# Kernel tuning notes

Measured on AMD Instinct MI355X. Metric: run time of the kernel, lower is better.

The kernel has to match this reference:

```python
import jax, jax.numpy as jnp
import numpy as np

B, T, C = 2, 2048, 1024
H, DK, OUT = 16, 64, 1024


def setup_inputs() -> dict:
    key = jax.random.key(0)
    k1, k2, k3, k4, k5 = jax.random.split(key, 5)
    glorot_qkv = (2.0 / (C + H * DK)) ** 0.5  # glorot_normal stddev for [C,H,DK]
    glorot_o = (2.0 / (H * DK + OUT)) ** 0.5
    return {
        "x": jax.random.normal(k1, (B, T, C), dtype=jnp.float32),
        "query_mat": jax.random.normal(k2, (C, H, DK), dtype=jnp.float32) * glorot_qkv,
        "key_mat": jax.random.normal(k3, (C, H, DK), dtype=jnp.float32) * glorot_qkv,
        "value_mat": jax.random.normal(k4, (C, H, DK), dtype=jnp.float32) * glorot_qkv,
        "linear_m1": jax.random.normal(k5, (H * DK, OUT), dtype=jnp.float32) * glorot_o,
    }


def reference(x, query_mat, key_mat, value_mat, linear_m1):
    # x: [B,T,C]; projections: [C,H,DK]
    q = jnp.einsum('btc,chd->bhtd', x, query_mat)
    k = jnp.einsum('btc,chd->bhtd', x, key_mat)
    v = jnp.einsum('btc,chd->bhtd', x, value_mat)
    d_k = query_mat.shape[-1]
    # NOTE: faithful to source, which MULTIPLIES by sqrt(d_k)
    w = jnp.einsum('bhtd,bhzd->bhtz', q, k) * (d_k ** 0.5)
    t = w.shape[-1]
    causal = jnp.tril(jnp.ones((t, t), dtype=bool))  # [T,T]
    w = jnp.where(causal, w, -jnp.inf)
    w = jax.nn.softmax(w, axis=-1)
    # dropout inactive (training=False)
    o = jnp.einsum('bhtz,bhzd->bhtd', w, v)
    o = o.transpose(0, 2, 1, 3).reshape(o.shape[0], o.shape[2], -1)  # [B,T,H*DK]
    return jnp.einsum('btc,cz->btz', o, linear_m1)
```

## Files before the change

kernel.cpp:

```cpp
#include <hip/hip_runtime.h>


typedef unsigned short u16;
typedef unsigned int u32;
typedef unsigned long long u64;
typedef __attribute__((ext_vector_type(8))) short bf16x8;
typedef __attribute__((ext_vector_type(4))) float f32x4;

__device__ inline u16 f2bf(float f) {
  union { float f; unsigned u; } v; v.f = f;
  unsigned r = v.u + 0x7FFFu + ((v.u >> 16) & 1u);
  return (u16)(r >> 16);
}
__device__ inline float bf2f(u16 h) {
  union { unsigned u; float f; } v; v.u = ((unsigned)h) << 16;
  return v.f;
}
__device__ inline void glds16(const u16* g, u16* s) {
  __builtin_amdgcn_global_load_lds(
      (const __attribute__((address_space(1))) u32*)g,
      (__attribute__((address_space(3))) u32*)s, 16, 0, 0);
}
#define MFMA __builtin_amdgcn_mfma_f32_16x16x32_bf16

__global__ __launch_bounds__(256) void prep(
    const float* __restrict__ x,
    const float* __restrict__ wq, const float* __restrict__ wk,
    const float* __restrict__ wv, const float* __restrict__ wo,
    u16* __restrict__ Xh, u16* __restrict__ Xl,
    u16* __restrict__ Wqh, u16* __restrict__ Wql,
    u16* __restrict__ Wkh, u16* __restrict__ Wkl,
    u16* __restrict__ Wvt, u16* __restrict__ Wot) {
  const int z = blockIdx.z;
  const int tid = threadIdx.x;
  if (z == 0) {
    const int bid = blockIdx.y * 32 + blockIdx.x;
#pragma unroll
    for (int k = 0; k < 4; k++) {
      int i = bid * 4096 + k * 1024 + tid * 4;
      float4 v = *(const float4*)(x + i);
      ushort4 h, l;
      h.x = f2bf(v.x); l.x = f2bf(v.x - bf2f(h.x));
      h.y = f2bf(v.y); l.y = f2bf(v.y - bf2f(h.y));
      h.z = f2bf(v.z); l.z = f2bf(v.z - bf2f(h.z));
      h.w = f2bf(v.w); l.w = f2bf(v.w - bf2f(h.w));
      *(ushort4*)(Xh + i) = h;
      *(ushort4*)(Xl + i) = l;
    }
    return;
  }
  __shared__ float tile[32][33];
  const float* W = (z == 1) ? wq : (z == 2) ? wk : (z == 3) ? wv : wo;
  const int bx = blockIdx.x * 32, by = blockIdx.y * 32;
  const int tx = tid & 31, ty = tid >> 5;
#pragma unroll
  for (int j = 0; j < 32; j += 8)
    tile[ty + j][tx] = W[(size_t)(by + ty + j) * 1024 + bx + tx];
  __syncthreads();
  if (z <= 2) {
    u16* Th = (z == 1) ? Wqh : Wkh;
    u16* Tl = (z == 1) ? Wql : Wkl;
#pragma unroll
    for (int j = 0; j < 32; j += 8) {
      float v = tile[tx][ty + j];
      u16 h = f2bf(v);
      size_t idx = (size_t)(bx + ty + j) * 1024 + by + tx;
      Th[idx] = h;
      Tl[idx] = f2bf(v - bf2f(h));
    }
  } else {
    u16* T = (z == 3) ? Wvt : Wot;
#pragma unroll
    for (int j = 0; j < 32; j += 8)
      T[(size_t)(bx + ty + j) * 1024 + by + tx] = f2bf(tile[tx][ty + j]);
  }
}

__global__ __launch_bounds__(256) void gemm_qkv(
    const u16* __restrict__ Xh, const u16* __restrict__ Xl,
    const u16* __restrict__ Wqh, const u16* __restrict__ Wql,
    const u16* __restrict__ Wkh, const u16* __restrict__ Wkl,
    const u16* __restrict__ Wvt,
    u16* __restrict__ Qh, u16* __restrict__ Ql,
    u16* __restrict__ Kh, u16* __restrict__ Kl,
    u16* __restrict__ Vt) {
  __shared__ u16 S[4][128][32];
  const int K = 1024;
  const int z = blockIdx.z;
  const bool split = (z < 2);
  const u16* Bh = (z == 0) ? Wqh : (z == 1) ? Wkh : Wvt;
  const u16* Bl = (z == 0) ? Wql : Wkl;
  const int tid = threadIdx.x;
  const int lane = tid & 63, wv = tid >> 6;
  const int quad = lane >> 4, lc = lane & 15;
  const int m0 = blockIdx.y * 128, n0 = blockIdx.x * 128;
  const int wm = (wv >> 1) * 64, wn = (wv & 1) * 64;
  const int lrow = lane >> 2, lk = (lane & 3) * 8;
  const u16* a0p = Xh + (size_t)(m0 + wv * 32 + lrow) * K + lk;
  const u16* a1p = a0p + 16 * K;
  const u16* al0p = Xl + (size_t)(m0 + wv * 32 + lrow) * K + lk;
  const u16* al1p = al0p + 16 * K;
  const u16* b0p = Bh + (size_t)(n0 + wv * 32 + lrow) * K + lk;
  const u16* b1p = b0p + 16 * K;
  const u16* bl0p = split ? (Bl + (size_t)(n0 + wv * 32 + lrow) * K + lk) : b0p;
  const u16* bl1p = bl0p + 16 * K;
  u16* sA0 = &S[0][wv * 32][0];      u16* sA1 = &S[0][wv * 32 + 16][0];
  u16* sAl0 = &S[1][wv * 32][0];     u16* sAl1 = &S[1][wv * 32 + 16][0];
  u16* sB0 = &S[2][wv * 32][0];      u16* sB1 = &S[2][wv * 32 + 16][0];
  u16* sBl0 = &S[3][wv * 32][0];     u16* sBl1 = &S[3][wv * 32 + 16][0];
  f32x4 acc[4][4];
#pragma unroll
  for (int i = 0; i < 4; i++)
#pragma unroll
    for (int j = 0; j < 4; j++) acc[i][j] = (f32x4){0.f, 0.f, 0.f, 0.f};
  for (int kc = 0; kc < K; kc += 32) {
    __syncthreads();
    glds16(a0p + kc, sA0); glds16(a1p + kc, sA1);
    glds16(b0p + kc, sB0); glds16(b1p + kc, sB1);
    if (split) {
      glds16(al0p + kc, sAl0); glds16(al1p + kc, sAl1);
      glds16(bl0p + kc, sBl0); glds16(bl1p + kc, sBl1);
    }
    __syncthreads();
    bf16x8 ah[4], al[4];
#pragma unroll
    for (int mt = 0; mt < 4; mt++)
      ah[mt] = *(const bf16x8*)&S[0][wm + mt * 16 + lc][quad * 8];
    if (split) {
#pragma unroll
      for (int mt = 0; mt < 4; mt++)
        al[mt] = *(const bf16x8*)&S[1][wm + mt * 16 + lc][quad * 8];
    }
#pragma unroll
    for (int nt = 0; nt < 4; nt++) {
      bf16x8 bfh = *(const bf16x8*)&S[2][wn + nt * 16 + lc][quad * 8];
#pragma unroll
      for (int mt = 0; mt < 4; mt++)
        acc[mt][nt] = MFMA(ah[mt], bfh, acc[mt][nt], 0, 0, 0);
      if (split) {
        bf16x8 bfl = *(const bf16x8*)&S[3][wn + nt * 16 + lc][quad * 8];
#pragma unroll
        for (int mt = 0; mt < 4; mt++) {
          acc[mt][nt] = MFMA(ah[mt], bfl, acc[mt][nt], 0, 0, 0);
          acc[mt][nt] = MFMA(al[mt], bfh, acc[mt][nt], 0, 0, 0);
        }
      }
    }
  }
  const int rb = quad * 4;
  if (z == 2) {
#pragma unroll
    for (int mt = 0; mt < 4; mt++)
#pragma unroll
      for (int nt = 0; nt < 4; nt++)
#pragma unroll
        for (int r = 0; r < 4; r++) {
          int m = m0 + wm + mt * 16 + rb + r, n = n0 + wn + nt * 16 + lc;
          int b = m >> 11, t = m & 2047, h = n >> 6, d = n & 63;
          Vt[((size_t)(b * 16 + h) * 64 + d) * 2048 + t] = f2bf(acc[mt][nt][r]);
        }
  } else {
    u16* Ch = (z == 0) ? Qh : Kh;
    u16* Cl = (z == 0) ? Ql : Kl;
    const float scale = (z == 0) ? 8.0f : 1.0f;
#pragma unroll
    for (int mt = 0; mt < 4; mt++)
#pragma unroll
      for (int nt = 0; nt < 4; nt++)
#pragma unroll
        for (int r = 0; r < 4; r++) {
          int m = m0 + wm + mt * 16 + rb + r, n = n0 + wn + nt * 16 + lc;
          int b = m >> 11, t = m & 2047, h = n >> 6, d = n & 63;
          float v = acc[mt][nt][r] * scale;
          u16 hv = f2bf(v);
          size_t idx = ((size_t)(b * 16 + h) * 2048 + t) * 64 + d;
          Ch[idx] = hv;
          Cl[idx] = f2bf(v - bf2f(hv));
        }
  }
}

__global__ __launch_bounds__(256) void gemm_out(const u16* __restrict__ A,
                                                const u16* __restrict__ Bt,
                                                float* __restrict__ C) {
  __shared__ u16 Sa[64][32], Sb[128][32];
  const int K = 1024, N = 1024;
  const int tid = threadIdx.x;
  const int lane = tid & 63, wv = tid >> 6;
  const int quad = lane >> 4, lc = lane & 15;
  const int m0 = blockIdx.y * 64, n0 = blockIdx.x * 128;
  const int wm = (wv >> 1) * 32, wn = (wv & 1) * 64;
  const int lrow = lane >> 2, lk = (lane & 3) * 8;
  const u16* ap = A + (size_t)(m0 + wv * 16 + lrow) * K + lk;
  const u16* b0p = Bt + (size_t)(n0 + wv * 32 + lrow) * K + lk;
  const u16* b1p = b0p + 16 * K;
  u16* sA = &Sa[wv * 16][0];
  u16* sB0 = &Sb[wv * 32][0];
  u16* sB1 = &Sb[wv * 32 + 16][0];
  f32x4 acc[2][4];
#pragma unroll
  for (int i = 0; i < 2; i++)
#pragma unroll
    for (int j = 0; j < 4; j++) acc[i][j] = (f32x4){0.f, 0.f, 0.f, 0.f};
  for (int kc = 0; kc < K; kc += 32) {
    __syncthreads();
    glds16(ap + kc, sA);
    glds16(b0p + kc, sB0);
    glds16(b1p + kc, sB1);
    __syncthreads();
    bf16x8 ah[2];
#pragma unroll
    for (int mt = 0; mt < 2; mt++)
      ah[mt] = *(const bf16x8*)&Sa[wm + mt * 16 + lc][quad * 8];
#pragma unroll
    for (int nt = 0; nt < 4; nt++) {
      bf16x8 bfh = *(const bf16x8*)&Sb[wn + nt * 16 + lc][quad * 8];
#pragma unroll
      for (int mt = 0; mt < 2; mt++)
        acc[mt][nt] = MFMA(ah[mt], bfh, acc[mt][nt], 0, 0, 0);
    }
  }
#pragma unroll
  for (int mt = 0; mt < 2; mt++)
#pragma unroll
    for (int nt = 0; nt < 4; nt++)
#pragma unroll
      for (int r = 0; r < 4; r++)
        C[(size_t)(m0 + wm + mt * 16 + quad * 4 + r) * N + n0 + wn + nt * 16 + lc] =
            acc[mt][nt][r];
}

__global__ __launch_bounds__(256, 2) void attn(const u16* __restrict__ Qh,
                                               const u16* __restrict__ Ql,
                                               const u16* __restrict__ Kh,
                                               const u16* __restrict__ Kl,
                                               const u16* __restrict__ Vt,
                                               u16* __restrict__ O16) {
  __shared__ u16 Khs[2][64][64], Kls[2][64][64], Vs[2][64][64];
  __shared__ u16 Ps[4][16][72];
  const int tid = threadIdx.x;
  const int lane = tid & 63, w = tid >> 6;
  const int quad = lane >> 4, lc = lane & 15;
  const int i = blockIdx.x;
  const int bh = i & 31;
  const int qb = 31 - (i >> 5);
  const int ng = qb + 1;
  const int tq = qb * 64 + w * 16 + lc;
  const size_t kbase = (size_t)bh * 2048 * 64;
  const size_t vbase = (size_t)bh * 64 * 2048;
  const size_t qoff = kbase + (size_t)tq * 64 + quad * 8;
  bf16x8 qh0 = *(const bf16x8*)(Qh + qoff);
  bf16x8 qh1 = *(const bf16x8*)(Qh + qoff + 32);
  bf16x8 ql0 = *(const bf16x8*)(Ql + qoff);
  bf16x8 ql1 = *(const bf16x8*)(Ql + qoff + 32);
  const int srow = lane >> 3;
  const int scol = (lane & 7) ^ srow;
  const u16* kg0 = Kh + kbase + (size_t)(w * 16 + srow) * 64 + scol * 8;
  const u16* lg0 = Kl + kbase + (size_t)(w * 16 + srow) * 64 + scol * 8;
  const u16* vg0 = Vt + vbase + (size_t)(w * 16 + srow) * 2048 + scol * 8;

  float mi = -3.0e38f, li = 0.f;
  f32x4 o[4];
#pragma unroll
  for (int d = 0; d < 4; d++) o[d] = (f32x4){0.f, 0.f, 0.f, 0.f};
  const int rx = lc & 7;

  {
    glds16(kg0, &Khs[0][w * 16][0]); glds16(kg0 + 8 * 64, &Khs[0][w * 16 + 8][0]);
    glds16(lg0, &Kls[0][w * 16][0]); glds16(lg0 + 8 * 64, &Kls[0][w * 16 + 8][0]);
    glds16(vg0, &Vs[0][w * 16][0]);  glds16(vg0 + 8 * 2048, &Vs[0][w * 16 + 8][0]);
  }
  for (int g = 0; g < ng; g++) {
    const int buf = g & 1;
    const int z0 = g * 64;
    __syncthreads();
    if (g + 1 < ng) {
      const int zn = (g + 1) * 64;
      const int nb = buf ^ 1;
      glds16(kg0 + (size_t)zn * 64, &Khs[nb][w * 16][0]);
      glds16(kg0 + (size_t)zn * 64 + 8 * 64, &Khs[nb][w * 16 + 8][0]);
      glds16(lg0 + (size_t)zn * 64, &Kls[nb][w * 16][0]);
      glds16(lg0 + (size_t)zn * 64 + 8 * 64, &Kls[nb][w * 16 + 8][0]);
      glds16(vg0 + zn, &Vs[nb][w * 16][0]);
      glds16(vg0 + zn + 8 * 2048, &Vs[nb][w * 16 + 8][0]);
    }
    f32x4 s[4];
#pragma unroll
    for (int tt = 0; tt < 4; tt++) {
      const int R = tt * 16 + lc;
      bf16x8 kh0 = *(const bf16x8*)&Khs[buf][R][(quad ^ rx) * 8];
      bf16x8 kh1 = *(const bf16x8*)&Khs[buf][R][((4 + quad) ^ rx) * 8];
      bf16x8 kl0 = *(const bf16x8*)&Kls[buf][R][(quad ^ rx) * 8];
      bf16x8 kl1 = *(const bf16x8*)&Kls[buf][R][((4 + quad) ^ rx) * 8];
      f32x4 sv = (f32x4){0.f, 0.f, 0.f, 0.f};
      sv = MFMA(kh0, qh0, sv, 0, 0, 0);
      sv = MFMA(kh1, qh1, sv, 0, 0, 0);
      sv = MFMA(kh0, ql0, sv, 0, 0, 0);
      sv = MFMA(kh1, ql1, sv, 0, 0, 0);
      sv = MFMA(kl0, qh0, sv, 0, 0, 0);
      sv = MFMA(kl1, qh1, sv, 0, 0, 0);
      s[tt] = sv;
    }
    if (g == ng - 1) {
#pragma unroll
      for (int tt = 0; tt < 4; tt++)
#pragma unroll
        for (int r = 0; r < 4; r++)
          if (z0 + tt * 16 + quad * 4 + r > tq) s[tt][r] = -3.0e38f;
    }
    float smax = -3.0e38f;
#pragma unroll
    for (int tt = 0; tt < 4; tt++)
#pragma unroll
      for (int r = 0; r < 4; r++) smax = fmaxf(smax, s[tt][r]);
    smax = fmaxf(smax, __shfl_xor(smax, 16));
    smax = fmaxf(smax, __shfl_xor(smax, 32));
    float mnew = fmaxf(mi, smax);
    float alpha = __expf(mi - mnew);
    mi = mnew;
    float rs = 0.f;
#pragma unroll
    for (int tt = 0; tt < 4; tt++) {
      union { u16 h[4]; u64 d; } pk;
#pragma unroll
      for (int r = 0; r < 4; r++) {
        float p = __expf(s[tt][r] - mnew);
        rs += p;
        pk.h[r] = f2bf(p);
      }
      *(u64*)&Ps[w][lc][tt * 16 + quad * 4] = pk.d;
    }
    li = li * alpha + rs;
#pragma unroll
    for (int d = 0; d < 4; d++) o[d] *= alpha;
    bf16x8 pf0 = *(const bf16x8*)&Ps[w][lc][quad * 8];
    bf16x8 pf1 = *(const bf16x8*)&Ps[w][lc][32 + quad * 8];
#pragma unroll
    for (int dd = 0; dd < 4; dd++) {
      const int R = dd * 16 + lc;
      bf16x8 va0 = *(const bf16x8*)&Vs[buf][R][(quad ^ rx) * 8];
      bf16x8 va1 = *(const bf16x8*)&Vs[buf][R][((4 + quad) ^ rx) * 8];
      o[dd] = MFMA(va0, pf0, o[dd], 0, 0, 0);
      o[dd] = MFMA(va1, pf1, o[dd], 0, 0, 0);
    }
  }
  li += __shfl_xor(li, 16);
  li += __shfl_xor(li, 32);
  const float rli = 1.0f / li;
  const int b = bh >> 4, hh = bh & 15;
  const size_t obase = ((size_t)(b * 2048 + tq)) * 1024 + hh * 64 + quad * 4;
#pragma unroll
  for (int dd = 0; dd < 4; dd++) {
    ushort4 ov;
    ov.x = f2bf(o[dd][0] * rli);
    ov.y = f2bf(o[dd][1] * rli);
    ov.z = f2bf(o[dd][2] * rli);
    ov.w = f2bf(o[dd][3] * rli);
    *(ushort4*)&O16[obase + dd * 16] = ov;
  }
}

extern "C" void kernel_launch(void* const* d_in, const int* in_sizes, int n_in,
                              void* d_out, int out_size, void* d_ws, size_t ws_size,
                              hipStream_t stream) {
  const float* x  = (const float*)d_in[0];
  const float* wq = (const float*)d_in[1];
  const float* wk = (const float*)d_in[2];
  const float* wv = (const float*)d_in[3];
  const float* wo = (const float*)d_in[4];

  char* w = (char*)d_ws;
  const size_t MB = 1u << 20;
  u16* Xh  = (u16*)(w + 0 * MB);
  u16* Xl  = (u16*)(w + 8 * MB);
  u16* Wqh = (u16*)(w + 16 * MB);
  u16* Wql = (u16*)(w + 18 * MB);
  u16* Wkh = (u16*)(w + 20 * MB);
  u16* Wkl = (u16*)(w + 22 * MB);
  u16* Wvt = (u16*)(w + 24 * MB);
  u16* Wot = (u16*)(w + 26 * MB);
  u16* Qhb = (u16*)(w + 28 * MB);
  u16* Qlb = (u16*)(w + 36 * MB);
  u16* Khb = (u16*)(w + 44 * MB);
  u16* Klb = (u16*)(w + 52 * MB);
  u16* Vtb = (u16*)(w + 60 * MB);
  u16* O16 = (u16*)(w + 0 * MB);

  hipLaunchKernelGGL(prep, dim3(32, 32, 5), dim3(256), 0, stream,
                     x, wq, wk, wv, wo, Xh, Xl, Wqh, Wql, Wkh, Wkl, Wvt, Wot);

  hipLaunchKernelGGL(gemm_qkv, dim3(8, 32, 3), dim3(256), 0, stream,
                     Xh, Xl, Wqh, Wql, Wkh, Wkl, Wvt, Qhb, Qlb, Khb, Klb, Vtb);

  hipLaunchKernelGGL(attn, dim3(1024), dim3(256), 0, stream,
                     Qhb, Qlb, Khb, Klb, Vtb, O16);

  hipLaunchKernelGGL(gemm_out, dim3(8, 64), dim3(256), 0, stream, O16, Wot, (float*)d_out);
}
```

Before: 214.3 us.

## Pair causal query blocks per workgroup and software-pipeline PV behind QK

Each attention workgroup now handles two query blocks, qb and 31-qb, so every block does the same amount of causal work and the grid halves to 512. The PV MFMA for the previous key tile is deferred and issued after the current tile's QK MFMAs, with V fragments held in registers. This is meant to overlap softmax latency with matrix work and to remove the tail imbalance of causal scheduling. It raises register pressure through the held V fragments and leaves fewer workgroups to spread across the CUs.

```diff
diff --git a/kernel.cpp b/kernel.cpp
--- a/kernel.cpp
+++ b/kernel.cpp
@@ -241,122 +241,146 @@
   const int tid = threadIdx.x;
   const int lane = tid & 63, w = tid >> 6;
   const int quad = lane >> 4, lc = lane & 15;
-  const int i = blockIdx.x;
-  const int bh = i & 31;
-  const int qb = 31 - (i >> 5);
-  const int ng = qb + 1;
-  const int tq = qb * 64 + w * 16 + lc;
+  const int j = blockIdx.x;
+  const int bh = j & 31;
+  const int pr = j >> 5;
   const size_t kbase = (size_t)bh * 2048 * 64;
   const size_t vbase = (size_t)bh * 64 * 2048;
-  const size_t qoff = kbase + (size_t)tq * 64 + quad * 8;
-  bf16x8 qh0 = *(const bf16x8*)(Qh + qoff);
-  bf16x8 qh1 = *(const bf16x8*)(Qh + qoff + 32);
-  bf16x8 ql0 = *(const bf16x8*)(Ql + qoff);
-  bf16x8 ql1 = *(const bf16x8*)(Ql + qoff + 32);
   const int srow = lane >> 3;
   const int scol = (lane & 7) ^ srow;
+  const int rx = lc & 7;
   const u16* kg0 = Kh + kbase + (size_t)(w * 16 + srow) * 64 + scol * 8;
   const u16* lg0 = Kl + kbase + (size_t)(w * 16 + srow) * 64 + scol * 8;
   const u16* vg0 = Vt + vbase + (size_t)(w * 16 + srow) * 2048 + scol * 8;
-
-  float mi = -3.0e38f, li = 0.f;
-  f32x4 o[4];
-#pragma unroll
-  for (int d = 0; d < 4; d++) o[d] = (f32x4){0.f, 0.f, 0.f, 0.f};
-  const int rx = lc & 7;
-
-  {
+  const int b = bh >> 4, hh = bh & 15;
+
+#pragma unroll 1
+  for (int sb = 0; sb < 2; sb++) {
+    const int qb = sb ? pr : 31 - pr;
+    const int ng = qb + 1;
+    const int tq = qb * 64 + w * 16 + lc;
+    const size_t qoff = kbase + (size_t)tq * 64 + quad * 8;
+    bf16x8 qh0 = *(const bf16x8*)(Qh + qoff);
+    bf16x8 qh1 = *(const bf16x8*)(Qh + qoff + 32);
+    bf16x8 ql0 = *(const bf16x8*)(Ql + qoff);
+    bf16x8 ql1 = *(const bf16x8*)(Ql + qoff + 32);
+    float mi = -3.0e38f, li = 0.f;
+    f32x4 o[4];
+#pragma unroll
+    for (int d = 0; d < 4; d++) o[d] = (f32x4){0.f, 0.f, 0.f, 0.f};
+    bf16x8 vprev[4][2];
+    __syncthreads();
     glds16(kg0, &Khs[0][w * 16][0]); glds16(kg0 + 8 * 64, &Khs[0][w * 16 + 8][0]);
     glds16(lg0, &Kls[0][w * 16][0]); glds16(lg0 + 8 * 64, &Kls[0][w * 16 + 8][0]);
     glds16(vg0, &Vs[0][w * 16][0]);  glds16(vg0 + 8 * 2048, &Vs[0][w * 16 + 8][0]);
-  }
-  for (int g = 0; g < ng; g++) {
-    const int buf = g & 1;
-    const int z0 = g * 64;
-    __syncthreads();
-    if (g + 1 < ng) {
-      const int zn = (g + 1) * 64;
-      const int nb = buf ^ 1;
-      glds16(kg0 + (size_t)zn * 64, &Khs[nb][w * 16][0]);
-      glds16(kg0 + (size_t)zn * 64 + 8 * 64, &Khs[nb][w * 16 + 8][0]);
-      glds16(lg0 + (size_t)zn * 64, &Kls[nb][w * 16][0]);
-      glds16(lg0 + (size_t)zn * 64 + 8 * 64, &Kls[nb][w * 16 + 8][0]);
-      glds16(vg0 + zn, &Vs[nb][w * 16][0]);
-      glds16(vg0 + zn + 8 * 2048, &Vs[nb][w * 16 + 8][0]);
-    }
-    f32x4 s[4];
-#pragma unroll
-    for (int tt = 0; tt < 4; tt++) {
-      const int R = tt * 16 + lc;
-      bf16x8 kh0 = *(const bf16x8*)&Khs[buf][R][(quad ^ rx) * 8];
-      bf16x8 kh1 = *(const bf16x8*)&Khs[buf][R][((4 + quad) ^ rx) * 8];
-      bf16x8 kl0 = *(const bf16x8*)&Kls[buf][R][(quad ^ rx) * 8];
-      bf16x8 kl1 = *(const bf16x8*)&Kls[buf][R][((4 + quad) ^ rx) * 8];
-      f32x4 sv = (f32x4){0.f, 0.f, 0.f, 0.f};
-      sv = MFMA(kh0, qh0, sv, 0, 0, 0);
-      sv = MFMA(kh1, qh1, sv, 0, 0, 0);
-      sv = MFMA(kh0, ql0, sv, 0, 0, 0);
-      sv = MFMA(kh1, ql1, sv, 0, 0, 0);
-      sv = MFMA(kl0, qh0, sv, 0, 0, 0);
-      sv = MFMA(kl1, qh1, sv, 0, 0, 0);
-      s[tt] = sv;
-    }
-    if (g == ng - 1) {
+#pragma unroll 1
+    for (int g = 0; g < ng; g++) {
+      const int buf = g & 1;
+      const int z0 = g * 64;
+      __syncthreads();
+      if (g + 1 < ng) {
+        const int zn = (g + 1) * 64;
+        const int nb = buf ^ 1;
+        glds16(kg0 + (size_t)zn * 64, &Khs[nb][w * 16][0]);
+        glds16(kg0 + (size_t)zn * 64 + 8 * 64, &Khs[nb][w * 16 + 8][0]);
+        glds16(lg0 + (size_t)zn * 64, &Kls[nb][w * 16][0]);
+        glds16(lg0 + (size_t)zn * 64 + 8 * 64, &Kls[nb][w * 16 + 8][0]);
+        glds16(vg0 + zn, &Vs[nb][w * 16][0]);
+        glds16(vg0 + zn + 8 * 2048, &Vs[nb][w * 16 + 8][0]);
+      }
+      bf16x8 vb[4][2];
+#pragma unroll
+      for (int dd = 0; dd < 4; dd++) {
+        const int R = dd * 16 + lc;
+        vb[dd][0] = *(const bf16x8*)&Vs[buf][R][(quad ^ rx) * 8];
+        vb[dd][1] = *(const bf16x8*)&Vs[buf][R][((4 + quad) ^ rx) * 8];
+      }
+      f32x4 s[4];
+#pragma unroll
+      for (int tt = 0; tt < 4; tt++) {
+        const int R = tt * 16 + lc;
+        bf16x8 kh0 = *(const bf16x8*)&Khs[buf][R][(quad ^ rx) * 8];
+        bf16x8 kh1 = *(const bf16x8*)&Khs[buf][R][((4 + quad) ^ rx) * 8];
+        bf16x8 kl0 = *(const bf16x8*)&Kls[buf][R][(quad ^ rx) * 8];
+        bf16x8 kl1 = *(const bf16x8*)&Kls[buf][R][((4 + quad) ^ rx) * 8];
+        f32x4 sv = (f32x4){0.f, 0.f, 0.f, 0.f};
+        sv = MFMA(kh0, qh0, sv, 0, 0, 0);
+        sv = MFMA(kh1, qh1, sv, 0, 0, 0);
+        sv = MFMA(kh0, ql0, sv, 0, 0, 0);
+        sv = MFMA(kh1, ql1, sv, 0, 0, 0);
+        sv = MFMA(kl0, qh0, sv, 0, 0, 0);
+        sv = MFMA(kl1, qh1, sv, 0, 0, 0);
+        s[tt] = sv;
+      }
+      if (g > 0) {
+        bf16x8 pf0 = *(const bf16x8*)&Ps[w][lc][quad * 8];
+        bf16x8 pf1 = *(const bf16x8*)&Ps[w][lc][32 + quad * 8];
+#pragma unroll
+        for (int dd = 0; dd < 4; dd++) {
+          o[dd] = MFMA(vprev[dd][0], pf0, o[dd], 0, 0, 0);
+          o[dd] = MFMA(vprev[dd][1], pf1, o[dd], 0, 0, 0);
+        }
+      }
+      if (g == ng - 1) {
+#pragma unroll
+        for (int tt = 0; tt < 4; tt++)
+#pragma unroll
+          for (int r = 0; r < 4; r++)
+            if (z0 + tt * 16 + quad * 4 + r > tq) s[tt][r] = -3.0e38f;
+      }
+      float smax = -3.0e38f;
 #pragma unroll
       for (int tt = 0; tt < 4; tt++)
 #pragma unroll
-        for (int r = 0; r < 4; r++)
-          if (z0 + tt * 16 + quad * 4 + r > tq) s[tt][r] = -3.0e38f;
-    }
-    float smax = -3.0e38f;
-#pragma unroll
-    for (int tt = 0; tt < 4; tt++)
-#pragma unroll
-      for (int r = 0; r < 4; r++) smax = fmaxf(smax, s[tt][r]);
-    smax = fmaxf(smax, __shfl_xor(smax, 16));
-    smax = fmaxf(smax, __shfl_xor(smax, 32));
-    float mnew = fmaxf(mi, smax);
-    float alpha = __expf(mi - mnew);
-    mi = mnew;
-    float rs = 0.f;
-#pragma unroll
-    for (int tt = 0; tt < 4; tt++) {
-      union { u16 h[4]; u64 d; } pk;
-#pragma unroll
-      for (int r = 0; r < 4; r++) {
-        float p = __expf(s[tt][r] - mnew);
-        rs += p;
-        pk.h[r] = f2bf(p);
-      }
-      *(u64*)&Ps[w][lc][tt * 16 + quad * 4] = pk.d;
-    }
-    li = li * alpha + rs;
-#pragma unroll
-    for (int d = 0; d < 4; d++) o[d] *= alpha;
-    bf16x8 pf0 = *(const bf16x8*)&Ps[w][lc][quad * 8];
-    bf16x8 pf1 = *(const bf16x8*)&Ps[w][lc][32 + quad * 8];
+        for (int r = 0; r < 4; r++) smax = fmaxf(smax, s[tt][r]);
+      smax = fmaxf(smax, __shfl_xor(smax, 16));
+      smax = fmaxf(smax, __shfl_xor(smax, 32));
+      float mnew = fmaxf(mi, smax);
+      float alpha = __expf(mi - mnew);
+      mi = mnew;
+#pragma unroll
+      for (int d = 0; d < 4; d++) o[d] *= alpha;
+      float rs = 0.f;
+#pragma unroll
+      for (int tt = 0; tt < 4; tt++) {
+        union { u16 h[4]; u64 d; } pk;
+#pragma unroll
+        for (int r = 0; r < 4; r++) {
+          float p = __expf(s[tt][r] - mnew);
+          rs += p;
+          pk.h[r] = f2bf(p);
+        }
+        *(u64*)&Ps[w][lc][tt * 16 + quad * 4] = pk.d;
+      }
+      li = li * alpha + rs;
+#pragma unroll
+      for (int dd = 0; dd < 4; dd++) {
+        vprev[dd][0] = vb[dd][0];
+        vprev[dd][1] = vb[dd][1];
+      }
+    }
+    {
+      bf16x8 pf0 = *(const bf16x8*)&Ps[w][lc][quad * 8];
+      bf16x8 pf1 = *(const bf16x8*)&Ps[w][lc][32 + quad * 8];
+#pragma unroll
+      for (int dd = 0; dd < 4; dd++) {
+        o[dd] = MFMA(vprev[dd][0], pf0, o[dd], 0, 0, 0);
+        o[dd] = MFMA(vprev[dd][1], pf1, o[dd], 0, 0, 0);
+      }
+    }
+    li += __shfl_xor(li, 16);
+    li += __shfl_xor(li, 32);
+    const float rli = 1.0f / li;
+    const size_t obase = ((size_t)(b * 2048 + tq)) * 1024 + hh * 64 + quad * 4;
 #pragma unroll
     for (int dd = 0; dd < 4; dd++) {
-      const int R = dd * 16 + lc;
-      bf16x8 va0 = *(const bf16x8*)&Vs[buf][R][(quad ^ rx) * 8];
-      bf16x8 va1 = *(const bf16x8*)&Vs[buf][R][((4 + quad) ^ rx) * 8];
-      o[dd] = MFMA(va0, pf0, o[dd], 0, 0, 0);
-      o[dd] = MFMA(va1, pf1, o[dd], 0, 0, 0);
-    }
-  }
-  li += __shfl_xor(li, 16);
-  li += __shfl_xor(li, 32);
-  const float rli = 1.0f / li;
-  const int b = bh >> 4, hh = bh & 15;
-  const size_t obase = ((size_t)(b * 2048 + tq)) * 1024 + hh * 64 + quad * 4;
-#pragma unroll
-  for (int dd = 0; dd < 4; dd++) {
-    ushort4 ov;
-    ov.x = f2bf(o[dd][0] * rli);
-    ov.y = f2bf(o[dd][1] * rli);
-    ov.z = f2bf(o[dd][2] * rli);
-    ov.w = f2bf(o[dd][3] * rli);
-    *(ushort4*)&O16[obase + dd * 16] = ov;
+      ushort4 ov;
+      ov.x = f2bf(o[dd][0] * rli);
+      ov.y = f2bf(o[dd][1] * rli);
+      ov.z = f2bf(o[dd][2] * rli);
+      ov.w = f2bf(o[dd][3] * rli);
+      *(ushort4*)&O16[obase + dd * 16] = ov;
+    }
   }
 }
 
@@ -392,7 +416,7 @@
   hipLaunchKernelGGL(gemm_qkv, dim3(8, 32, 3), dim3(256), 0, stream,
                      Xh, Xl, Wqh, Wql, Wkh, Wkl, Wvt, Qhb, Qlb, Khb, Klb, Vtb);
 
-  hipLaunchKernelGGL(attn, dim3(1024), dim3(256), 0, stream,
+  hipLaunchKernelGGL(attn, dim3(512), dim3(256), 0, stream,
                      Qhb, Qlb, Khb, Klb, Vtb, O16);
 
   hipLaunchKernelGGL(gemm_out, dim3(8, 64), dim3(256), 0, stream, O16, Wot, (float*)d_out);
```

Measured after the change: 219.5 us. 2.4% more time.

## Fuse Q and K projections into one block sharing the X tiles

Applied to the files above, without the earlier changes.

The QKV projection GEMM now computes Q and K together in the same block (grid z of 2 instead of 3), so the X hi/lo tiles are loaded into LDS once and reused for both weight matrices. This removes one redundant pass over X and one set of blocks. The cost is twice the accumulator registers (32 f32x4 per thread), larger LDS (6 tiles), a hint of 2 blocks per CU via launch bounds that may force spills, and imbalance between the heavy Q/K blocks and the light V blocks.

```diff
diff --git a/kernel.cpp b/kernel.cpp
--- a/kernel.cpp
+++ b/kernel.cpp
@@ -76,7 +76,7 @@
   }
 }
 
-__global__ __launch_bounds__(256) void gemm_qkv(
+__global__ __launch_bounds__(256, 2) void gemm_qkv(
     const u16* __restrict__ Xh, const u16* __restrict__ Xl,
     const u16* __restrict__ Wqh, const u16* __restrict__ Wql,
     const u16* __restrict__ Wkh, const u16* __restrict__ Wkl,
@@ -84,71 +84,83 @@
     u16* __restrict__ Qh, u16* __restrict__ Ql,
     u16* __restrict__ Kh, u16* __restrict__ Kl,
     u16* __restrict__ Vt) {
-  __shared__ u16 S[4][128][32];
+  __shared__ u16 S[6][128][32];
   const int K = 1024;
-  const int z = blockIdx.z;
-  const bool split = (z < 2);
-  const u16* Bh = (z == 0) ? Wqh : (z == 1) ? Wkh : Wvt;
-  const u16* Bl = (z == 0) ? Wql : Wkl;
+  const bool qk = (blockIdx.z == 0);
   const int tid = threadIdx.x;
   const int lane = tid & 63, wv = tid >> 6;
   const int quad = lane >> 4, lc = lane & 15;
   const int m0 = blockIdx.y * 128, n0 = blockIdx.x * 128;
   const int wm = (wv >> 1) * 64, wn = (wv & 1) * 64;
   const int lrow = lane >> 2, lk = (lane & 3) * 8;
-  const u16* a0p = Xh + (size_t)(m0 + wv * 32 + lrow) * K + lk;
-  const u16* a1p = a0p + 16 * K;
-  const u16* al0p = Xl + (size_t)(m0 + wv * 32 + lrow) * K + lk;
-  const u16* al1p = al0p + 16 * K;
-  const u16* b0p = Bh + (size_t)(n0 + wv * 32 + lrow) * K + lk;
-  const u16* b1p = b0p + 16 * K;
-  const u16* bl0p = split ? (Bl + (size_t)(n0 + wv * 32 + lrow) * K + lk) : b0p;
-  const u16* bl1p = bl0p + 16 * K;
-  u16* sA0 = &S[0][wv * 32][0];      u16* sA1 = &S[0][wv * 32 + 16][0];
-  u16* sAl0 = &S[1][wv * 32][0];     u16* sAl1 = &S[1][wv * 32 + 16][0];
-  u16* sB0 = &S[2][wv * 32][0];      u16* sB1 = &S[2][wv * 32 + 16][0];
-  u16* sBl0 = &S[3][wv * 32][0];     u16* sBl1 = &S[3][wv * 32 + 16][0];
-  f32x4 acc[4][4];
+  const size_t arow = (size_t)(m0 + wv * 32 + lrow) * K + lk;
+  const size_t brow = (size_t)(n0 + wv * 32 + lrow) * K + lk;
+  const u16* a0p = Xh + arow;
+  const u16* al0p = Xl + arow;
+  const u16* bq0p = (qk ? Wqh : Wvt) + brow;
+  const u16* bql0p = (qk ? Wql : Wvt) + brow;
+  const u16* bk0p = (qk ? Wkh : Wvt) + brow;
+  const u16* bkl0p = (qk ? Wkl : Wvt) + brow;
+  u16* sA0 = &S[0][wv * 32][0];   u16* sA1 = &S[0][wv * 32 + 16][0];
+  u16* sAl0 = &S[1][wv * 32][0];  u16* sAl1 = &S[1][wv * 32 + 16][0];
+  u16* sQ0 = &S[2][wv * 32][0];   u16* sQ1 = &S[2][wv * 32 + 16][0];
+  u16* sQl0 = &S[3][wv * 32][0];  u16* sQl1 = &S[3][wv * 32 + 16][0];
+  u16* sK0 = &S[4][wv * 32][0];   u16* sK1 = &S[4][wv * 32 + 16][0];
+  u16* sKl0 = &S[5][wv * 32][0];  u16* sKl1 = &S[5][wv * 32 + 16][0];
+  f32x4 accq[4][4], acck[4][4];
 #pragma unroll
   for (int i = 0; i < 4; i++)
 #pragma unroll
-    for (int j = 0; j < 4; j++) acc[i][j] = (f32x4){0.f, 0.f, 0.f, 0.f};
+    for (int j = 0; j < 4; j++) {
+      accq[i][j] = (f32x4){0.f, 0.f, 0.f, 0.f};
+      acck[i][j] = (f32x4){0.f, 0.f, 0.f, 0.f};
+    }
   for (int kc = 0; kc < K; kc += 32) {
     __syncthreads();
-    glds16(a0p + kc, sA0); glds16(a1p + kc, sA1);
-    glds16(b0p + kc, sB0); glds16(b1p + kc, sB1);
-    if (split) {
-      glds16(al0p + kc, sAl0); glds16(al1p + kc, sAl1);
-      glds16(bl0p + kc, sBl0); glds16(bl1p + kc, sBl1);
+    glds16(a0p + kc, sA0);  glds16(a0p + 16 * K + kc, sA1);
+    glds16(bq0p + kc, sQ0); glds16(bq0p + 16 * K + kc, sQ1);
+    if (qk) {
+      glds16(al0p + kc, sAl0);  glds16(al0p + 16 * K + kc, sAl1);
+      glds16(bql0p + kc, sQl0); glds16(bql0p + 16 * K + kc, sQl1);
+      glds16(bk0p + kc, sK0);   glds16(bk0p + 16 * K + kc, sK1);
+      glds16(bkl0p + kc, sKl0); glds16(bkl0p + 16 * K + kc, sKl1);
     }
     __syncthreads();
     bf16x8 ah[4], al[4];
 #pragma unroll
     for (int mt = 0; mt < 4; mt++)
       ah[mt] = *(const bf16x8*)&S[0][wm + mt * 16 + lc][quad * 8];
-    if (split) {
+    if (qk) {
 #pragma unroll
       for (int mt = 0; mt < 4; mt++)
         al[mt] = *(const bf16x8*)&S[1][wm + mt * 16 + lc][quad * 8];
     }
 #pragma unroll
     for (int nt = 0; nt < 4; nt++) {
-      bf16x8 bfh = *(const bf16x8*)&S[2][wn + nt * 16 + lc][quad * 8];
+      bf16x8 bqh = *(const bf16x8*)&S[2][wn + nt * 16 + lc][quad * 8];
 #pragma unroll
       for (int mt = 0; mt < 4; mt++)
-        acc[mt][nt] = MFMA(ah[mt], bfh, acc[mt][nt], 0, 0, 0);
-      if (split) {
-        bf16x8 bfl = *(const bf16x8*)&S[3][wn + nt * 16 + lc][quad * 8];
+        accq[mt][nt] = MFMA(ah[mt], bqh, accq[mt][nt], 0, 0, 0);
+      if (qk) {
+        bf16x8 bql = *(const bf16x8*)&S[3][wn + nt * 16 + lc][quad * 8];
 #pragma unroll
         for (int mt = 0; mt < 4; mt++) {
-          acc[mt][nt] = MFMA(ah[mt], bfl, acc[mt][nt], 0, 0, 0);
-          acc[mt][nt] = MFMA(al[mt], bfh, acc[mt][nt], 0, 0, 0);
+          accq[mt][nt] = MFMA(ah[mt], bql, accq[mt][nt], 0, 0, 0);
+          accq[mt][nt] = MFMA(al[mt], bqh, accq[mt][nt], 0, 0, 0);
+        }
+        bf16x8 bkh = *(const bf16x8*)&S[4][wn + nt * 16 + lc][quad * 8];
+        bf16x8 bkl = *(const bf16x8*)&S[5][wn + nt * 16 + lc][quad * 8];
+#pragma unroll
+        for (int mt = 0; mt < 4; mt++) {
+          acck[mt][nt] = MFMA(ah[mt], bkh, acck[mt][nt], 0, 0, 0);
+          acck[mt][nt] = MFMA(ah[mt], bkl, acck[mt][nt], 0, 0, 0);
+          acck[mt][nt] = MFMA(al[mt], bkh, acck[mt][nt], 0, 0, 0);
         }
       }
     }
   }
   const int rb = quad * 4;
-  if (z == 2) {
+  if (!qk) {
 #pragma unroll
     for (int mt = 0; mt < 4; mt++)
 #pragma unroll
@@ -157,12 +169,9 @@
         for (int r = 0; r < 4; r++) {
           int m = m0 + wm + mt * 16 + rb + r, n = n0 + wn + nt * 16 + lc;
           int b = m >> 11, t = m & 2047, h = n >> 6, d = n & 63;
-          Vt[((size_t)(b * 16 + h) * 64 + d) * 2048 + t] = f2bf(acc[mt][nt][r]);
+          Vt[((size_t)(b * 16 + h) * 64 + d) * 2048 + t] = f2bf(accq[mt][nt][r]);
         }
   } else {
-    u16* Ch = (z == 0) ? Qh : Kh;
-    u16* Cl = (z == 0) ? Ql : Kl;
-    const float scale = (z == 0) ? 8.0f : 1.0f;
 #pragma unroll
     for (int mt = 0; mt < 4; mt++)
 #pragma unroll
@@ -171,11 +180,15 @@
         for (int r = 0; r < 4; r++) {
           int m = m0 + wm + mt * 16 + rb + r, n = n0 + wn + nt * 16 + lc;
           int b = m >> 11, t = m & 2047, h = n >> 6, d = n & 63;
-          float v = acc[mt][nt][r] * scale;
-          u16 hv = f2bf(v);
           size_t idx = ((size_t)(b * 16 + h) * 2048 + t) * 64 + d;
-          Ch[idx] = hv;
-          Cl[idx] = f2bf(v - bf2f(hv));
+          float vq = accq[mt][nt][r] * 8.0f;
+          u16 hq = f2bf(vq);
+          Qh[idx] = hq;
+          Ql[idx] = f2bf(vq - bf2f(hq));
+          float vk = acck[mt][nt][r];
+          u16 hk = f2bf(vk);
+          Kh[idx] = hk;
+          Kl[idx] = f2bf(vk - bf2f(hk));
         }
   }
 }
@@ -389,7 +402,7 @@
   hipLaunchKernelGGL(prep, dim3(32, 32, 5), dim3(256), 0, stream,
                      x, wq, wk, wv, wo, Xh, Xl, Wqh, Wql, Wkh, Wkl, Wvt, Wot);
 
-  hipLaunchKernelGGL(gemm_qkv, dim3(8, 32, 3), dim3(256), 0, stream,
+  hipLaunchKernelGGL(gemm_qkv, dim3(8, 32, 2), dim3(256), 0, stream,
                      Xh, Xl, Wqh, Wql, Wkh, Wkl, Wvt, Qhb, Qlb, Khb, Klb, Vtb);
 
   hipLaunchKernelGGL(attn, dim3(1024), dim3(256), 0, stream,
```

Measured after the change: 235.9 us. +10.1%, slower.
